# Kernel optimization log

Hardware: AMD Instinct MI355X
Metric: run time of the kernel (lower is better)

## Reference

```python
import jax, jax.numpy as jnp
import numpy as np
import math

N, E, MUL = 10000, 160000, 128
D = MUL * 4  # 128x0e (128) + 128x1o (384) = 512
NEURONS = 32
EDGE_ATTR_DIM = 32
WEIGHT_NUMEL = 4 * MUL  # 4 uvu tensor-product paths, 128 weights each


def ssp(x):
    return jax.nn.softplus(x) - math.log(2.0)


def irrep_linear(x, W0, b0, W1):
    # o3.Linear on 128x0e+128x1o: mixes mul channels within each irrep, fan-in normalized,
    # bias only on scalar (0e) block.
    s = x[:, :MUL] @ (W0 / jnp.sqrt(MUL)) + b0
    v = x[:, MUL:].reshape(-1, MUL, 3)
    v = jnp.einsum('num,uv->nvm', v, W1) / jnp.sqrt(MUL)
    return jnp.concatenate([s, v.reshape(-1, MUL * 3)], axis=-1)


def inner_product(a, b):
    # InnerProduct: uuu channel-wise irrep inner product, 1/sqrt(dim) normalized
    s = a[:, :MUL] * b[:, :MUL]
    va = a[:, MUL:].reshape(-1, MUL, 3)
    vb = b[:, MUL:].reshape(-1, MUL, 3)
    v = jnp.einsum('num,num->nu', va, vb) / jnp.sqrt(3.0)
    return jnp.concatenate([s, v], axis=-1)


def norm_gate(x, W1, b1, W2, b2):
    # NormGate: per-channel norms of l>0 irreps -> MLP gates -> gate l>0 channels
    v = x[:, MUL:].reshape(-1, MUL, 3)
    norm_v = jnp.sqrt(jnp.sum(v * v, axis=-1) + 1e-12)      # [n, 128]
    f0 = jnp.concatenate([x[:, :MUL], norm_v], axis=-1)     # [n, 256]
    g = jax.nn.silu(f0 @ W1 + b1) @ W2 + b2                 # [n, 256]
    gated = v * g[:, MUL:, None]
    return jnp.concatenate([g[:, :MUL], gated.reshape(-1, MUL * 3)], axis=-1)


def mlp2(x, Wa, Wb):
    # e3nn FullyConnectedNet: fan-in normalized, ssp nonlinearity on hidden layer only
    return ssp(x @ (Wa / jnp.sqrt(Wa.shape[0]))) @ (Wb / jnp.sqrt(Wb.shape[0]))


def setup_inputs():
    key = jax.random.key(0)
    ks = jax.random.split(key, 20)
    r = lambda i, shp: jax.random.normal(ks[i], shp, dtype=jnp.float32)
    return {
        'x': r(0, (N, D)),
        'edge_index': jax.random.randint(ks[1], (2, E), 0, N, dtype=jnp.int32),
        'edge_attr': jax.random.uniform(ks[2], (E, EDGE_ATTR_DIM), dtype=jnp.float32),
        'edge_sh': r(3, (E, 4)),
        'Wp0': r(4, (MUL, MUL)), 'bp0': jnp.zeros((MUL,), jnp.float32), 'Wp1': r(5, (MUL, MUL)),
        'ngW1': r(6, (2 * MUL, 2 * MUL)) / 16.0, 'ngb1': jnp.zeros((2 * MUL,), jnp.float32),
        'ngW2': r(7, (2 * MUL, 2 * MUL)) / 16.0, 'ngb2': jnp.zeros((2 * MUL,), jnp.float32),
        'Wn0': r(8, (MUL, MUL)), 'bn0': jnp.zeros((MUL,), jnp.float32), 'Wn1': r(9, (MUL, MUL)),
        'fcnW1': r(10, (EDGE_ATTR_DIM, NEURONS)), 'fcnW2': r(11, (NEURONS, WEIGHT_NUMEL)),
        'l0W1': r(12, (3 * MUL, NEURONS)), 'l0W2': r(13, (NEURONS, WEIGHT_NUMEL)),
        'Wo0': r(14, (MUL, MUL)), 'bo0': jnp.zeros((MUL,), jnp.float32), 'Wo1': r(15, (MUL, MUL)),
    }


def reference(x, edge_index, edge_attr, edge_sh, Wp0, bp0, Wp1, ngW1, ngb1, ngW2, ngb2,
              Wn0, bn0, Wn1, fcnW1, fcnW2, l0W1, l0W2, Wo0, bo0, Wo1):
    edge_dst, edge_src = edge_index[0], edge_index[1]
    # invariant edge descriptor s0 from pre-linear + inner product
    pre_x = irrep_linear(x, Wp0, bp0, Wp1)
    ip = inner_product(pre_x[edge_dst], pre_x[edge_src])[:, MUL:]             # [E,128]
    s0 = jnp.concatenate([pre_x[edge_dst][:, :MUL], pre_x[edge_src][:, :MUL], ip], axis=-1)  # [E,384]
    # norm-gate + linear on node features
    x = norm_gate(x, ngW1, ngb1, ngW2, ngb2)
    x = irrep_linear(x, Wn0, bn0, Wn1)
    self_x = x
    # per-edge tensor-product weights: fc_node(edge_attr) * layer_l0(s0)
    w = mlp2(edge_attr, fcnW1, fcnW2) * mlp2(s0, l0W1, l0W2)                   # [E,512]
    w1, w2, w3, w4 = w[:, :MUL], w[:, MUL:2 * MUL], w[:, 2 * MUL:3 * MUL], w[:, 3 * MUL:]
    xs = x[edge_src]
    xs0 = xs[:, :MUL]                     # [E,128]
    xs1 = xs[:, MUL:].reshape(E, MUL, 3)  # [E,128,3]
    sh0 = edge_sh[:, 0:1]
    sh1 = edge_sh[:, 1:4]
    # uvu CG tensor product paths: 0ex0e->0e, 0ex1o->1o, 1ox0e->1o, 1ox1o->0e
    c0, c1 = 0.5, jnp.sqrt(3.0) / 2.0  # path norm sqrt(ir_out.dim / n_paths)
    out0 = c0 * (w1 * xs0 * sh0 + w4 * jnp.einsum('eum,em->eu', xs1, sh1) / jnp.sqrt(3.0))
    out1 = c1 * (w2[:, :, None] * xs0[:, :, None] * sh1[:, None, :]
                 + w3[:, :, None] * xs1 * sh0[:, :, None])
    edge_feat = jnp.concatenate([out0, out1.reshape(E, MUL * 3)], axis=-1)     # [E,512]
    # scatter-aggregate to destination nodes, residual, output linear
    out = jax.ops.segment_sum(edge_feat, edge_dst, num_segments=N)
    out = out + self_x
    return irrep_linear(out, Wo0, bo0, Wo1)
```

## Files before the change

kernel.cpp:

```cpp
#include <hip/hip_runtime.h>
#include <hip/hip_fp16.h>
#include <math.h>

#define NN 10000
#define EE 160000
#define DPB 8

#define RS128 0.08838834764831845f
#define RS384 0.05103103630798287f
#define RS32  0.17677669529663687f
#define R3    0.57735026918962576f
#define C1V   0.86602540378443865f

typedef _Float16 half8 __attribute__((ext_vector_type(8)));
typedef _Float16 half4 __attribute__((ext_vector_type(4)));
typedef float f32x4 __attribute__((ext_vector_type(4)));

__device__ __forceinline__ float sspf(float x) {
    return fmaxf(x, 0.0f) + log1pf(__expf(-fabsf(x))) - 0.69314718055994530942f;
}

__device__ __forceinline__ void packone(const float* __restrict__ W,
                                        _Float16* __restrict__ P,
                                        int K, int N, int off) {
    const int KS = K >> 5;
    int j = off & 7, lane = (off >> 3) & 63, rest = off >> 9;
    int ks = rest % KS, ct = rest / KS;
    int k = ks * 32 + ((lane >> 4) << 3) + j;
    int c = ct * 16 + (lane & 15);
    P[off] = (_Float16)W[k * N + c];
}

__global__ __launch_bounds__(256) void k_packall(
    const float* __restrict__ Wp0, const float* __restrict__ Wp1,
    const float* __restrict__ Wn0, const float* __restrict__ Wn1,
    const float* __restrict__ Wo0, const float* __restrict__ Wo1,
    const float* __restrict__ ngW1, const float* __restrict__ ngW2,
    const float* __restrict__ l0W1, const float* __restrict__ fcnW1,
    const float* __restrict__ fcnW2, const float* __restrict__ l0W2,
    _Float16* __restrict__ pWp0, _Float16* __restrict__ pWp1,
    _Float16* __restrict__ pWn0, _Float16* __restrict__ pWn1,
    _Float16* __restrict__ pWo0, _Float16* __restrict__ pWo1,
    _Float16* __restrict__ png1, _Float16* __restrict__ png2,
    _Float16* __restrict__ pWc, _Float16* __restrict__ pWa,
    _Float16* __restrict__ Wf_t, _Float16* __restrict__ Wl_t,
    _Float16* __restrict__ pWab, int* __restrict__ degz) {
    int idx = blockIdx.x * 256 + threadIdx.x;
    if (idx < 98304) {
        int seg = idx >> 14, off = idx & 16383;
        if (seg == 0) packone(Wp0, pWp0, 128, 128, off);
        else if (seg == 1) packone(Wp1, pWp1, 128, 128, off);
        else if (seg == 2) packone(Wn0, pWn0, 128, 128, off);
        else if (seg == 3) packone(Wn1, pWn1, 128, 128, off);
        else if (seg == 4) packone(Wo0, pWo0, 128, 128, off);
        else packone(Wo1, pWo1, 128, 128, off);
    } else if (idx < 229376) {
        int r = idx - 98304;
        if (r < 65536) packone(ngW1, png1, 256, 256, r);
        else packone(ngW2, png2, 256, 256, r - 65536);
    } else if (idx < 233472) {
        packone(l0W1 + 256 * 32, pWc, 128, 32, idx - 229376);
    } else if (idx < 234496) {
        packone(fcnW1, pWa, 32, 32, idx - 233472);
    } else if (idx < 250880) {
        int off = idx - 234496;
        int k = off & 31, c = off >> 5;
        Wf_t[c * 32 + k] = (_Float16)fcnW2[k * 512 + c];
        Wl_t[c * 32 + k] = (_Float16)l0W2[k * 512 + c];
    } else if (idx < 259072) {
        int off = idx - 250880;
        int j = off & 7, lane = (off >> 3) & 63, rest = off >> 9;
        int ks = rest & 3, ct = rest >> 2;
        int k = ks * 32 + ((lane >> 4) << 3) + j;
        int c = ct * 16 + (lane & 15);
        pWab[off] = (_Float16)((c < 32) ? l0W1[k * 32 + c]
                                        : l0W1[(128 + k) * 32 + (c - 32)]);
    } else if (idx < 279072) {
        degz[idx - 259072] = 0;
    }
}

__global__ __launch_bounds__(256) void k_irrep_m(
    const float* __restrict__ X, const _Float16* __restrict__ pW0,
    const float* __restrict__ b0, const _Float16* __restrict__ pW1,
    float* __restrict__ out) {
    __shared__ _Float16 Xr[4][16][136];
    const int t = threadIdx.x, lane = t & 63, w = t >> 6;
    const int nb = blockIdx.x * 16;
    for (int idx = t; idx < 16 * 128; idx += 256) {
        int n = idx >> 7, c4 = idx & 127;
        const float4 v = *(const float4*)(X + (size_t)(nb + n) * 512 + 4 * c4);
        float vals[4] = {v.x, v.y, v.z, v.w};
        int c = 4 * c4;
#pragma unroll
        for (int j = 0; j < 4; ++j) {
            int cc = c + j;
            if (cc < 128) Xr[0][n][cc] = (_Float16)vals[j];
            else { int d = cc - 128; Xr[1 + d % 3][n][d / 3] = (_Float16)vals[j]; }
        }
    }
    __syncthreads();
    const _Float16* pW = (w == 0) ? pW0 : pW1;
    const int row16 = lane & 15, kg = lane >> 4;
    f32x4 acc[8];
    const f32x4 zero = {0.0f, 0.0f, 0.0f, 0.0f};
#pragma unroll
    for (int ct = 0; ct < 8; ++ct) acc[ct] = zero;
    for (int ks = 0; ks < 4; ++ks) {
        const half8 a = *(const half8*)&Xr[w][row16][ks * 32 + kg * 8];
#pragma unroll
        for (int ct = 0; ct < 8; ++ct) {
            const half8 b = *(const half8*)(pW + (((ct * 4 + ks) * 64 + lane) << 3));
            acc[ct] = __builtin_amdgcn_mfma_f32_16x16x32_f16(a, b, acc[ct], 0, 0, 0);
        }
    }
#pragma unroll
    for (int ct = 0; ct < 8; ++ct) {
        const int col = ct * 16 + row16;
        const float bb = (w == 0) ? b0[col] : 0.0f;
#pragma unroll
        for (int r = 0; r < 4; ++r) {
            const int node = nb + kg * 4 + r;
            const float val = acc[ct][r] * RS128 + bb;
            if (w == 0) out[(size_t)node * 512 + col] = val;
            else out[(size_t)node * 512 + 128 + 3 * col + (w - 1)] = val;
        }
    }
}

__global__ __launch_bounds__(256) void k_node(
    const float* __restrict__ X,
    const _Float16* __restrict__ pWp0, const float* __restrict__ bp0,
    const _Float16* __restrict__ pWp1, const _Float16* __restrict__ pWab,
    const _Float16* __restrict__ png1, const float* __restrict__ ngb1,
    const _Float16* __restrict__ png2, const float* __restrict__ ngb2,
    const _Float16* __restrict__ pWn0, const float* __restrict__ bn0,
    const _Float16* __restrict__ pWn1,
    _Float16* __restrict__ prexv_h, float* __restrict__ pAB,
    _Float16* __restrict__ selfx_h) {
    __shared__ _Float16 f0h[16][264];
    __shared__ _Float16 t1h[16][264];
    __shared__ _Float16 xvh[3][16][136];
    __shared__ _Float16 pvh[3][16][136];
    const int t = threadIdx.x, lane = t & 63, w = t >> 6;
    const int nb = blockIdx.x * 16;
    const int row16 = lane & 15, kg = lane >> 4;
    const f32x4 zero = {0.0f, 0.0f, 0.0f, 0.0f};

    for (int idx = t; idx < 16 * 128; idx += 256) {
        int n = idx >> 7, c4 = idx & 127;
        const float4 v = *(const float4*)(X + (size_t)(nb + n) * 512 + 4 * c4);
        float vals[4] = {v.x, v.y, v.z, v.w};
        int c = 4 * c4;
#pragma unroll
        for (int j = 0; j < 4; ++j) {
            int cc = c + j;
            if (cc < 128) f0h[n][cc] = (_Float16)vals[j];
            else { int d = cc - 128; xvh[d % 3][n][d / 3] = (_Float16)vals[j]; }
        }
    }
    __syncthreads();
    for (int idx = t; idx < 16 * 128; idx += 256) {
        int n = idx >> 7, u = idx & 127;
        float a = (float)xvh[0][n][u], b = (float)xvh[1][n][u], c = (float)xvh[2][n][u];
        f0h[n][128 + u] = (_Float16)sqrtf(fmaf(a, a, fmaf(b, b, fmaf(c, c, 1e-12f))));
    }
    __syncthreads();
    {
        const _Float16* pW = (w == 0) ? pWp0 : pWp1;
        f32x4 acc[8];
#pragma unroll
        for (int ct = 0; ct < 8; ++ct) acc[ct] = zero;
        for (int ks = 0; ks < 4; ++ks) {
            const half8 a = (w == 0)
                ? *(const half8*)&f0h[row16][ks * 32 + kg * 8]
                : *(const half8*)&xvh[w - 1][row16][ks * 32 + kg * 8];
#pragma unroll
            for (int ct = 0; ct < 8; ++ct) {
                const half8 b = *(const half8*)(pW + (((ct * 4 + ks) * 64 + lane) << 3));
                acc[ct] = __builtin_amdgcn_mfma_f32_16x16x32_f16(a, b, acc[ct], 0, 0, 0);
            }
        }
#pragma unroll
        for (int ct = 0; ct < 8; ++ct) {
            const int col = ct * 16 + row16;
            const float bb = (w == 0) ? bp0[col] : 0.0f;
#pragma unroll
            for (int r = 0; r < 4; ++r) {
                const int n = kg * 4 + r;
                const float val = acc[ct][r] * RS128 + bb;
                if (w == 0) t1h[n][col] = (_Float16)val;
                else pvh[w - 1][n][col] = (_Float16)val;
            }
        }
    }
    __syncthreads();
    {
        f32x4 acc = zero;
#pragma unroll
        for (int ks = 0; ks < 4; ++ks) {
            const half8 a = *(const half8*)&t1h[row16][ks * 32 + kg * 8];
            const half8 b = *(const half8*)(pWab + (((w * 4 + ks) * 64 + lane) << 3));
            acc = __builtin_amdgcn_mfma_f32_16x16x32_f16(a, b, acc, 0, 0, 0);
        }
        const int col = w * 16 + row16;
#pragma unroll
        for (int r = 0; r < 4; ++r)
            pAB[(size_t)(nb + kg * 4 + r) * 64 + col] = acc[r];
    }
    for (int idx = t; idx < 16 * 128; idx += 256) {
        int n = idx >> 7, u = idx & 127;
        half4 pv = {pvh[0][n][u], pvh[1][n][u], pvh[2][n][u], t1h[n][u]};
        *(half4*)(prexv_h + (size_t)(nb + n) * 512 + (u << 2)) = pv;
    }
    __syncthreads();
    {
        f32x4 acc[4];
#pragma unroll
        for (int i = 0; i < 4; ++i) acc[i] = zero;
        for (int ks = 0; ks < 8; ++ks) {
            const half8 a = *(const half8*)&f0h[row16][ks * 32 + kg * 8];
#pragma unroll
            for (int c2 = 0; c2 < 4; ++c2) {
                const int ct = 4 * w + c2;
                const half8 b = *(const half8*)(png1 + (((ct * 8 + ks) * 64 + lane) << 3));
                acc[c2] = __builtin_amdgcn_mfma_f32_16x16x32_f16(a, b, acc[c2], 0, 0, 0);
            }
        }
        __syncthreads();
#pragma unroll
        for (int c2 = 0; c2 < 4; ++c2) {
            const int col = (4 * w + c2) * 16 + row16;
            const float bb = ngb1[col];
#pragma unroll
            for (int r = 0; r < 4; ++r) {
                const float z = acc[c2][r] + bb;
                t1h[kg * 4 + r][col] = (_Float16)(z / (1.0f + __expf(-z)));
            }
        }
    }
    __syncthreads();
    {
        f32x4 acc[4];
#pragma unroll
        for (int i = 0; i < 4; ++i) acc[i] = zero;
        for (int ks = 0; ks < 8; ++ks) {
            const half8 a = *(const half8*)&t1h[row16][ks * 32 + kg * 8];
#pragma unroll
            for (int c2 = 0; c2 < 4; ++c2) {
                const int ct = 4 * w + c2;
                const half8 b = *(const half8*)(png2 + (((ct * 8 + ks) * 64 + lane) << 3));
                acc[c2] = __builtin_amdgcn_mfma_f32_16x16x32_f16(a, b, acc[c2], 0, 0, 0);
            }
        }
        __syncthreads();
#pragma unroll
        for (int c2 = 0; c2 < 4; ++c2) {
            const int col = (4 * w + c2) * 16 + row16;
            const float bb = ngb2[col];
#pragma unroll
            for (int r = 0; r < 4; ++r)
                f0h[kg * 4 + r][col] = (_Float16)(acc[c2][r] + bb);
        }
    }
    __syncthreads();
    for (int idx = t; idx < 16 * 128; idx += 256) {
        int n = idx >> 7, u = idx & 127;
        const _Float16 g = f0h[n][128 + u];
        xvh[0][n][u] = xvh[0][n][u] * g;
        xvh[1][n][u] = xvh[1][n][u] * g;
        xvh[2][n][u] = xvh[2][n][u] * g;
    }
    __syncthreads();
    {
        const _Float16* pw = (w == 0) ? pWn0 : pWn1;
        f32x4 acc[8];
#pragma unroll
        for (int ct = 0; ct < 8; ++ct) acc[ct] = zero;
        for (int ks = 0; ks < 4; ++ks) {
            const half8 a = (w == 0)
                ? *(const half8*)&f0h[row16][ks * 32 + kg * 8]
                : *(const half8*)&xvh[w - 1][row16][ks * 32 + kg * 8];
#pragma unroll
            for (int ct = 0; ct < 8; ++ct) {
                const half8 b = *(const half8*)(pw + (((ct * 4 + ks) * 64 + lane) << 3));
                acc[ct] = __builtin_amdgcn_mfma_f32_16x16x32_f16(a, b, acc[ct], 0, 0, 0);
            }
        }
#pragma unroll
        for (int ct = 0; ct < 8; ++ct) {
            const int col = ct * 16 + row16;
            const float bb = (w == 0) ? bn0[col] : 0.0f;
#pragma unroll
            for (int r = 0; r < 4; ++r) {
                const int n = kg * 4 + r;
                const float val = acc[ct][r] * RS128 + bb;
                if (w == 0) f0h[n][col] = (_Float16)val;
                else xvh[w - 1][n][col] = (_Float16)val;
            }
        }
    }
    __syncthreads();
    for (int idx = t; idx < 16 * 128; idx += 256) {
        int n = idx >> 7, u = idx & 127;
        half4 sx = {f0h[n][u], xvh[0][n][u], xvh[1][n][u], xvh[2][n][u]};
        *(half4*)(selfx_h + (size_t)(nb + n) * 512 + (u << 2)) = sx;
    }
}

__global__ __launch_bounds__(256) void k_deg(const int* __restrict__ ei, int* __restrict__ deg) {
    int e = blockIdx.x * 256 + threadIdx.x;
    if (e < EE) atomicAdd(&deg[ei[e]], 1);
}

__global__ __launch_bounds__(1024) void k_scan(const int* __restrict__ deg, int* __restrict__ row_ptr) {
    __shared__ int part[1024];
    const int t = threadIdx.x;
    const int base = t * 10;
    int loc[10];
    int s = 0;
#pragma unroll
    for (int i = 0; i < 10; ++i) {
        int idx = base + i;
        int d = (idx < NN) ? deg[idx] : 0;
        loc[i] = s;
        s += d;
    }
    part[t] = s;
    __syncthreads();
    for (int off = 1; off < 1024; off <<= 1) {
        int v = (t >= off) ? part[t - off] : 0;
        __syncthreads();
        part[t] += v;
        __syncthreads();
    }
    int excl = (t > 0) ? part[t - 1] : 0;
#pragma unroll
    for (int i = 0; i < 10; ++i) {
        int idx = base + i;
        if (idx <= NN) row_ptr[idx] = excl + loc[i];
    }
}

__global__ __launch_bounds__(256) void k_fill(const int* __restrict__ ei,
                                              const int* __restrict__ row_ptr,
                                              int* __restrict__ cursor,
                                              int* __restrict__ csr_eid) {
    int e = blockIdx.x * 256 + threadIdx.x;
    if (e < EE) {
        int d = ei[e];
        int pos = atomicAdd(&cursor[d], 1);
        csr_eid[row_ptr[d] + pos] = e;
    }
}

__global__ __launch_bounds__(256) void k_hidden_m(
    const _Float16* __restrict__ prexv_h, const float* __restrict__ pAB,
    const int* __restrict__ edge_index, const float* __restrict__ edge_attr,
    const int* __restrict__ csr_eid,
    const _Float16* __restrict__ pWc, const _Float16* __restrict__ pWa,
    __half* __restrict__ hh) {
    const int pb = blockIdx.x * 32;
    const int t = threadIdx.x, lane = t & 63, w = t >> 6;
    __shared__ _Float16 ipl[32][132];
    __shared__ _Float16 eal[32][36];
    __shared__ _Float16 h1o[32][32];
    __shared__ _Float16 hao[32][32];
    __shared__ int dsts[32], srcs[32], eids[32];

    if (t < 32) {
        const int id = csr_eid[pb + t];
        eids[t] = id;
        dsts[t] = edge_index[id];
        srcs[t] = edge_index[EE + id];
    }
    __syncthreads();
    for (int idx = t; idx < 32 * 32; idx += 256) {
        int e = idx >> 5, j = idx & 31;
        eal[e][j] = (_Float16)edge_attr[(size_t)eids[e] * 32 + j];
    }
    for (int idx = t; idx < 32 * 128; idx += 256) {
        int e = idx >> 7, u = idx & 127;
        const half4 pd = *(const half4*)(prexv_h + (size_t)dsts[e] * 512 + (u << 2));
        const half4 ps = *(const half4*)(prexv_h + (size_t)srcs[e] * 512 + (u << 2));
        const float ipv = (float)pd.x * (float)ps.x + (float)pd.y * (float)ps.y +
                          (float)pd.z * (float)ps.z;
        ipl[e][u] = (_Float16)(ipv * R3);
    }
    __syncthreads();

    const int row16 = lane & 15, kg = lane >> 4;
    const int mt = w >> 1, ct = w & 1;
    const int e0 = mt * 16;
    const f32x4 zero = {0.0f, 0.0f, 0.0f, 0.0f};
    const int kc = ct * 16 + row16;

    {
        f32x4 acc = zero;
#pragma unroll
        for (int ks = 0; ks < 4; ++ks) {
            const half8 a = *(const half8*)&ipl[e0 + row16][ks * 32 + kg * 8];
            const half8 b = *(const half8*)(pWc + (((ct * 4 + ks) * 64 + lane) << 3));
            acc = __builtin_amdgcn_mfma_f32_16x16x32_f16(a, b, acc, 0, 0, 0);
        }
#pragma unroll
        for (int r = 0; r < 4; ++r) {
            const int e = e0 + kg * 4 + r;
            const float v = acc[r] + pAB[(size_t)dsts[e] * 64 + kc]
                                   + pAB[(size_t)srcs[e] * 64 + 32 + kc];
            h1o[e][kc] = (_Float16)sspf(v * RS384);
        }
    }
    {
        const half8 a = *(const half8*)&eal[e0 + row16][kg * 8];
        const half8 b = *(const half8*)(pWa + ((ct * 64 + lane) << 3));
        f32x4 acc = __builtin_amdgcn_mfma_f32_16x16x32_f16(a, b, zero, 0, 0, 0);
#pragma unroll
        for (int r = 0; r < 4; ++r) {
            const int e = e0 + kg * 4 + r;
            hao[e][kc] = (_Float16)sspf((float)acc[r] * RS32);
        }
    }
    __syncthreads();
    for (int idx = t; idx < 32 * 32; idx += 256) {
        const int e = idx >> 5, j = idx & 31;
        unsigned vv;
        if (j < 16) {
            __half2 h2 = __halves2half2((__half)h1o[e][2 * j], (__half)h1o[e][2 * j + 1]);
            vv = *(unsigned*)&h2;
        } else {
            const int jj = j - 16;
            __half2 h2 = __halves2half2((__half)hao[e][2 * jj], (__half)hao[e][2 * jj + 1]);
            vv = *(unsigned*)&h2;
        }
        ((unsigned*)hh)[(size_t)(pb + e) * 32 + j] = vv;
    }
}

__global__ __launch_bounds__(512) void k_accum(
    const __half* __restrict__ hh, const _Float16* __restrict__ selfx_h,
    const int* __restrict__ edge_index, const float* __restrict__ edge_sh,
    const int* __restrict__ row_ptr, const int* __restrict__ csr_eid,
    const _Float16* __restrict__ Wf_t, const _Float16* __restrict__ Wl_t,
    float* __restrict__ outacc) {
    const int dst0 = blockIdx.x * DPB;
    const int t = threadIdx.x;
    const int lane = t & 63;
    const int wid = t >> 6;
    const int lcol = lane & 15;
    const int kg = lane >> 4;
    const int u = 16 * wid + lcol;
    const int koff = kg * 8;

    __shared__ __align__(16) _Float16 h1s[2][4][16][8];
    __shared__ __align__(16) _Float16 has[2][4][16][8];
    __shared__ float shl[2][16][4];
    __shared__ int srcs[2][16];
    __shared__ int cbeg[DPB], cne[DPB], cchk[DPB + 1];

    if (t < DPB) {
        const int b = row_ptr[dst0 + t];
        cbeg[t] = b;
        cne[t] = row_ptr[dst0 + t + 1] - b;
    }
    __syncthreads();
    if (t == 0) {
        int s = 0;
#pragma unroll
        for (int i = 0; i < DPB; ++i) { cchk[i] = s; s += max(1, (cne[i] + 15) >> 4); }
        cchk[DPB] = s;
    }
    half8 bf[4], bl[4];
#pragma unroll
    for (int q = 0; q < 4; ++q) {
        const int col = q * 128 + u;
        bf[q] = *(const half8*)(Wf_t + col * 32 + koff);
        bl[q] = *(const half8*)(Wl_t + col * 32 + koff);
    }
    __syncthreads();
    const int nc = cchk[DPB];
    const float inv32 = 1.0f / 32.0f;

    float acc0 = 0, acc1 = 0, acc2 = 0, acc3 = 0;

    unsigned rhh = 0;
    int rsrc = 0;
    float4 rsh = {0.0f, 0.0f, 0.0f, 0.0f};

    const int se = t >> 5, sw = t & 31;

    auto issue = [&](int ci) {
        int dd = 0;
        while (dd + 1 < DPB && ci >= cchk[dd + 1]) ++dd;
        const int c0 = (ci - cchk[dd]) << 4;
        const int ce = min(16, cne[dd] - c0);
        const int pos = cbeg[dd] + c0;
        rhh = (se < ce) ? ((const unsigned*)hh)[(size_t)(pos + se) * 32 + sw] : 0u;
        if (t < 16) {
            if (t < ce) {
                const int id = csr_eid[pos + t];
                rsrc = edge_index[EE + id];
                rsh = *(const float4*)(edge_sh + (size_t)id * 4);
            } else {
                rsrc = 0;
                rsh = make_float4(0.0f, 0.0f, 0.0f, 0.0f);
            }
        }
    };

    auto flush = [&](int dd) {
        acc0 += __shfl_xor(acc0, 16, 64); acc0 += __shfl_xor(acc0, 32, 64);
        acc1 += __shfl_xor(acc1, 16, 64); acc1 += __shfl_xor(acc1, 32, 64);
        acc2 += __shfl_xor(acc2, 16, 64); acc2 += __shfl_xor(acc2, 32, 64);
        acc3 += __shfl_xor(acc3, 16, 64); acc3 += __shfl_xor(acc3, 32, 64);
        if (lane < 16) {
            const size_t g = (size_t)(dst0 + dd) * 512;
            const half4 sx = *(const half4*)(selfx_h + g + (u << 2));
            outacc[g + u] = acc0 + (float)sx.x;
            outacc[g + 128 + 3 * u + 0] = acc1 + (float)sx.y;
            outacc[g + 128 + 3 * u + 1] = acc2 + (float)sx.z;
            outacc[g + 128 + 3 * u + 2] = acc3 + (float)sx.w;
        }
        acc0 = acc1 = acc2 = acc3 = 0;
    };

    issue(0);
    int cur = 0, cur_dd = 0;
    for (int ci = 0; ci < nc; ++ci) {
        if (sw < 16) ((unsigned*)h1s[cur])[(sw >> 2) * 64 + se * 4 + (sw & 3)] = rhh;
        else         ((unsigned*)has[cur])[((sw - 16) >> 2) * 64 + se * 4 + ((sw - 16) & 3)] = rhh;
        if (t < 16) {
            srcs[cur][t] = rsrc;
            shl[cur][t][0] = rsh.x; shl[cur][t][1] = rsh.y;
            shl[cur][t][2] = rsh.z; shl[cur][t][3] = rsh.w;
        }
        int dd = 0;
        while (dd + 1 < DPB && ci >= cchk[dd + 1]) ++dd;
        const int c0 = (ci - cchk[dd]) << 4;
        const int ce = min(16, cne[dd] - c0);
        if (ci + 1 < nc) issue(ci + 1);
        __syncthreads();
        if (dd != cur_dd) { flush(cur_dd); cur_dd = dd; }

        const half8 haf = *(const half8*)(&has[cur][kg][lcol][0]);
        const half8 h1f = *(const half8*)(&h1s[cur][kg][lcol][0]);
        const f32x4 zero = {0.0f, 0.0f, 0.0f, 0.0f};
        f32x4 A[4], B[4];
#pragma unroll
        for (int q = 0; q < 4; ++q) {
            A[q] = __builtin_amdgcn_mfma_f32_16x16x32_f16(haf, bf[q], zero, 0, 0, 0);
            B[q] = __builtin_amdgcn_mfma_f32_16x16x32_f16(h1f, bl[q], zero, 0, 0, 0);
        }
#pragma unroll
        for (int r = 0; r < 4; ++r) {
            const int e = kg * 4 + r;
            if (e < ce) {
                const float w1 = A[0][r] * B[0][r] * inv32;
                const float w2 = A[1][r] * B[1][r] * inv32;
                const float w3 = A[2][r] * B[2][r] * inv32;
                const float w4 = A[3][r] * B[3][r] * inv32;
                const int src = srcs[cur][e];
                const float sh0 = shl[cur][e][0], s1x = shl[cur][e][1];
                const float s1y = shl[cur][e][2], s1z = shl[cur][e][3];
                const half4 sx = *(const half4*)(selfx_h + (size_t)src * 512 + (u << 2));
                const float xs0 = (float)sx.x;
                const float xv0 = (float)sx.y;
                const float xv1 = (float)sx.z;
                const float xv2 = (float)sx.w;
                const float dv = xv0 * s1x + xv1 * s1y + xv2 * s1z;
                acc0 += 0.5f * (w1 * xs0 * sh0 + w4 * dv * R3);
                acc1 += C1V * (w2 * xs0 * s1x + w3 * xv0 * sh0);
                acc2 += C1V * (w2 * xs0 * s1y + w3 * xv1 * sh0);
                acc3 += C1V * (w2 * xs0 * s1z + w3 * xv2 * sh0);
            }
        }
        cur ^= 1;
    }
    flush(cur_dd);
}

extern "C" void kernel_launch(void* const* d_in, const int* in_sizes, int n_in,
                              void* d_out, int out_size, void* d_ws, size_t ws_size,
                              hipStream_t stream) {
    const float* x = (const float*)d_in[0];
    const int* edge_index = (const int*)d_in[1];
    const float* edge_attr = (const float*)d_in[2];
    const float* edge_sh = (const float*)d_in[3];
    const float* Wp0 = (const float*)d_in[4];
    const float* bp0 = (const float*)d_in[5];
    const float* Wp1 = (const float*)d_in[6];
    const float* ngW1 = (const float*)d_in[7];
    const float* ngb1 = (const float*)d_in[8];
    const float* ngW2 = (const float*)d_in[9];
    const float* ngb2 = (const float*)d_in[10];
    const float* Wn0 = (const float*)d_in[11];
    const float* bn0 = (const float*)d_in[12];
    const float* Wn1 = (const float*)d_in[13];
    const float* fcnW1 = (const float*)d_in[14];
    const float* fcnW2 = (const float*)d_in[15];
    const float* l0W1 = (const float*)d_in[16];
    const float* l0W2 = (const float*)d_in[17];
    const float* Wo0 = (const float*)d_in[18];
    const float* bo0 = (const float*)d_in[19];
    const float* Wo1 = (const float*)d_in[20];

    float* out = (float*)d_out;
    _Float16* prexv_h = (_Float16*)d_out;
    _Float16* selfx_h = (_Float16*)d_ws;
    int* deg = (int*)(selfx_h + (size_t)NN * 512);
    int* cursor = deg + NN;
    int* row_ptr = cursor + NN;
    int* csr_eid = row_ptr + NN + 1;
    float* pAB = (float*)(csr_eid + EE);
    __half* hh = (__half*)(pAB + (size_t)NN * 64);
    _Float16* Wf_t = (_Float16*)(hh + (size_t)EE * 64);
    _Float16* Wl_t = Wf_t + 512 * 32;
    _Float16* pWp0 = Wl_t + 512 * 32;
    _Float16* pWp1 = pWp0 + 128 * 128;
    _Float16* pWn0 = pWp1 + 128 * 128;
    _Float16* pWn1 = pWn0 + 128 * 128;
    _Float16* pWo0 = pWn1 + 128 * 128;
    _Float16* pWo1 = pWo0 + 128 * 128;
    _Float16* png1 = pWo1 + 128 * 128;
    _Float16* png2 = png1 + 256 * 256;
    _Float16* pWc  = png2 + 256 * 256;
    _Float16* pWa  = pWc + 128 * 32;
    _Float16* pWab = pWa + 32 * 32;

    k_packall<<<1091, 256, 0, stream>>>(Wp0, Wp1, Wn0, Wn1, Wo0, Wo1, ngW1, ngW2,
                                        l0W1, fcnW1, fcnW2, l0W2,
                                        pWp0, pWp1, pWn0, pWn1, pWo0, pWo1,
                                        png1, png2, pWc, pWa, Wf_t, Wl_t,
                                        pWab, deg);

    k_node<<<NN / 16, 256, 0, stream>>>(x, pWp0, bp0, pWp1, pWab,
                                        png1, ngb1, png2, ngb2, pWn0, bn0, pWn1,
                                        prexv_h, pAB, selfx_h);
    k_deg<<<EE / 256, 256, 0, stream>>>(edge_index, deg);
    k_scan<<<1, 1024, 0, stream>>>(deg, row_ptr);
    k_fill<<<EE / 256, 256, 0, stream>>>(edge_index, row_ptr, cursor, csr_eid);
    k_hidden_m<<<EE / 32, 256, 0, stream>>>(prexv_h, pAB, edge_index, edge_attr, csr_eid,
                                            pWc, pWa, hh);
    k_accum<<<NN / DPB, 512, 0, stream>>>(hh, selfx_h, edge_index, edge_sh, row_ptr, csr_eid,
                                          Wf_t, Wl_t, out);
    k_irrep_m<<<NN / 16, 256, 0, stream>>>(out, pWo0, bo0, pWo1, out);
}
```

Baseline: 254.2 us.

## Fuse output irrep linear into accumulation kernel epilogue

The final o3.Linear (k_irrep_m) now runs as an epilogue of k_accum. Per-destination aggregated features are staged in shared memory as fp16, and MFMA tiles compute the output linear directly, with rows beyond DPB masked. This removes one kernel launch and a full write and read of the 10000x512 fp32 intermediate through global memory. In exchange it adds shared memory per block, which may lower occupancy, and half of each 16-row MFMA tile is wasted because only 8 nodes are handled per block.

```diff
diff --git a/kernel.cpp b/kernel.cpp
--- a/kernel.cpp
+++ b/kernel.cpp
@@ -80,54 +80,6 @@
     }
 }
 
-__global__ __launch_bounds__(256) void k_irrep_m(
-    const float* __restrict__ X, const _Float16* __restrict__ pW0,
-    const float* __restrict__ b0, const _Float16* __restrict__ pW1,
-    float* __restrict__ out) {
-    __shared__ _Float16 Xr[4][16][136];
-    const int t = threadIdx.x, lane = t & 63, w = t >> 6;
-    const int nb = blockIdx.x * 16;
-    for (int idx = t; idx < 16 * 128; idx += 256) {
-        int n = idx >> 7, c4 = idx & 127;
-        const float4 v = *(const float4*)(X + (size_t)(nb + n) * 512 + 4 * c4);
-        float vals[4] = {v.x, v.y, v.z, v.w};
-        int c = 4 * c4;
-#pragma unroll
-        for (int j = 0; j < 4; ++j) {
-            int cc = c + j;
-            if (cc < 128) Xr[0][n][cc] = (_Float16)vals[j];
-            else { int d = cc - 128; Xr[1 + d % 3][n][d / 3] = (_Float16)vals[j]; }
-        }
-    }
-    __syncthreads();
-    const _Float16* pW = (w == 0) ? pW0 : pW1;
-    const int row16 = lane & 15, kg = lane >> 4;
-    f32x4 acc[8];
-    const f32x4 zero = {0.0f, 0.0f, 0.0f, 0.0f};
-#pragma unroll
-    for (int ct = 0; ct < 8; ++ct) acc[ct] = zero;
-    for (int ks = 0; ks < 4; ++ks) {
-        const half8 a = *(const half8*)&Xr[w][row16][ks * 32 + kg * 8];
-#pragma unroll
-        for (int ct = 0; ct < 8; ++ct) {
-            const half8 b = *(const half8*)(pW + (((ct * 4 + ks) * 64 + lane) << 3));
-            acc[ct] = __builtin_amdgcn_mfma_f32_16x16x32_f16(a, b, acc[ct], 0, 0, 0);
-        }
-    }
-#pragma unroll
-    for (int ct = 0; ct < 8; ++ct) {
-        const int col = ct * 16 + row16;
-        const float bb = (w == 0) ? b0[col] : 0.0f;
-#pragma unroll
-        for (int r = 0; r < 4; ++r) {
-            const int node = nb + kg * 4 + r;
-            const float val = acc[ct][r] * RS128 + bb;
-            if (w == 0) out[(size_t)node * 512 + col] = val;
-            else out[(size_t)node * 512 + 128 + 3 * col + (w - 1)] = val;
-        }
-    }
-}
-
 __global__ __launch_bounds__(256) void k_node(
     const float* __restrict__ X,
     const _Float16* __restrict__ pWp0, const float* __restrict__ bp0,
@@ -442,6 +394,8 @@
     const int* __restrict__ edge_index, const float* __restrict__ edge_sh,
     const int* __restrict__ row_ptr, const int* __restrict__ csr_eid,
     const _Float16* __restrict__ Wf_t, const _Float16* __restrict__ Wl_t,
+    const _Float16* __restrict__ pWo0, const float* __restrict__ bo0,
+    const _Float16* __restrict__ pWo1,
     float* __restrict__ outacc) {
     const int dst0 = blockIdx.x * DPB;
     const int t = threadIdx.x;
@@ -457,12 +411,15 @@
     __shared__ float shl[2][16][4];
     __shared__ int srcs[2][16];
     __shared__ int cbeg[DPB], cne[DPB], cchk[DPB + 1];
+    __shared__ __align__(16) _Float16 accP[4][16][136];
 
     if (t < DPB) {
         const int b = row_ptr[dst0 + t];
         cbeg[t] = b;
         cne[t] = row_ptr[dst0 + t + 1] - b;
     }
+    for (int idx = t; idx < 4 * 16 * 136; idx += 512)
+        ((_Float16*)accP)[idx] = (_Float16)0;
     __syncthreads();
     if (t == 0) {
         int s = 0;
@@ -516,10 +473,10 @@
         if (lane < 16) {
             const size_t g = (size_t)(dst0 + dd) * 512;
             const half4 sx = *(const half4*)(selfx_h + g + (u << 2));
-            outacc[g + u] = acc0 + (float)sx.x;
-            outacc[g + 128 + 3 * u + 0] = acc1 + (float)sx.y;
-            outacc[g + 128 + 3 * u + 1] = acc2 + (float)sx.z;
-            outacc[g + 128 + 3 * u + 2] = acc3 + (float)sx.w;
+            accP[0][dd][u] = (_Float16)(acc0 + (float)sx.x);
+            accP[1][dd][u] = (_Float16)(acc1 + (float)sx.y);
+            accP[2][dd][u] = (_Float16)(acc2 + (float)sx.z);
+            accP[3][dd][u] = (_Float16)(acc3 + (float)sx.w);
         }
         acc0 = acc1 = acc2 = acc3 = 0;
     };
@@ -577,6 +534,41 @@
         cur ^= 1;
     }
     flush(cur_dd);
+    __syncthreads();
+
+    {
+        const int m = wid >> 1;
+        const int ctg = (wid & 1) * 4;
+        const _Float16* pW = (m == 0) ? pWo0 : pWo1;
+        const f32x4 zero = {0.0f, 0.0f, 0.0f, 0.0f};
+        f32x4 acc[4];
+#pragma unroll
+        for (int i = 0; i < 4; ++i) acc[i] = zero;
+        for (int ks = 0; ks < 4; ++ks) {
+            const half8 a = *(const half8*)&accP[m][lcol][ks * 32 + koff];
+#pragma unroll
+            for (int c2 = 0; c2 < 4; ++c2) {
+                const int ct = ctg + c2;
+                const half8 b = *(const half8*)(pW + (((ct * 4 + ks) * 64 + lane) << 3));
+                acc[c2] = __builtin_amdgcn_mfma_f32_16x16x32_f16(a, b, acc[c2], 0, 0, 0);
+            }
+        }
+#pragma unroll
+        for (int c2 = 0; c2 < 4; ++c2) {
+            const int col = (ctg + c2) * 16 + lcol;
+            const float bb = (m == 0) ? bo0[col] : 0.0f;
+#pragma unroll
+            for (int r = 0; r < 4; ++r) {
+                const int row = kg * 4 + r;
+                if (row < DPB) {
+                    const size_t g = (size_t)(dst0 + row) * 512;
+                    const float val = acc[c2][r] * RS128 + bb;
+                    if (m == 0) outacc[g + col] = val;
+                    else outacc[g + 128 + 3 * col + (m - 1)] = val;
+                }
+            }
+        }
+    }
 }
 
 extern "C" void kernel_launch(void* const* d_in, const int* in_sizes, int n_in,
@@ -642,6 +634,5 @@
     k_hidden_m<<<EE / 32, 256, 0, stream>>>(prexv_h, pAB, edge_index, edge_attr, csr_eid,
                                             pWc, pWa, hh);
     k_accum<<<NN / DPB, 512, 0, stream>>>(hh, selfx_h, edge_index, edge_sh, row_ptr, csr_eid,
-                                          Wf_t, Wl_t, out);
-    k_irrep_m<<<NN / 16, 256, 0, stream>>>(out, pWo0, bo0, pWo1, out);
-}
+                                          Wf_t, Wl_t, pWo0, bo0, pWo1, out);
+}
```

Measured after the change: 254.4 us. Within noise of the previous version (+0.1%).
